# Optimization experiments

Measured on AMD Instinct MI355X. Metric: run time of the kernel, lower is better.

Reference implementation:

```python
import jax, jax.numpy as jnp
import numpy as np

N, L, S, D, H = 2, 2048, 2048, 128, 32  # batch, query len, state len, hidden_dim(=head dim), num_heads


def setup_inputs() -> dict:
    key = jax.random.key(0)
    ks = jax.random.split(key, 8)
    return {
        "query": jax.random.normal(ks[0], (N, L, D), dtype=jnp.float32),
        "states": jax.random.normal(ks[1], (N, S, D), dtype=jnp.float32),
        "Wk": jax.random.normal(ks[2], (H, D, D), dtype=jnp.float32) * 0.05,
        "bk": jax.random.normal(ks[3], (H, D), dtype=jnp.float32) * 0.05,
        "Wv": jax.random.normal(ks[4], (H, D, D), dtype=jnp.float32) * 0.05,
        "bv": jax.random.normal(ks[5], (H, D), dtype=jnp.float32) * 0.05,
        "Wc": jax.random.normal(ks[6], (H * D, D), dtype=jnp.float32) * 0.02,
        "bc": jax.random.normal(ks[7], (D,), dtype=jnp.float32) * 0.02,
    }


def reference(query, states, Wk, bk, Wv, bv, Wc, bc):
    # Per-head key/value projections (Attention.keys_mlp / values_mlp), batched over heads.
    K = jnp.einsum('nsd,hdk->nhsk', states, Wk) + bk[None, :, None, :]  # [N,H,S,D]
    V = jnp.einsum('nsd,hdk->nhsk', states, Wv) + bv[None, :, None, :]  # [N,H,S,D]
    scale = jnp.sqrt(jnp.asarray(K.shape[-1], query.dtype))
    logits = jnp.einsum('nld,nhsd->nhls', query, K) / scale            # [N,H,L,S]
    # Original detaches attention scores (softmax(...).detach()).
    A = jax.lax.stop_gradient(jax.nn.softmax(logits, axis=-1))
    ctx = jnp.einsum('nhls,nhsd->nhld', A, V)                          # [N,H,L,D]
    n, h, l, d = ctx.shape
    ctx = ctx.transpose(0, 2, 1, 3).reshape(n, l, h * d)               # concat heads -> [N,L,H*D]
    return ctx @ Wc + bc                                               # context_transform
```

## Files before the change

kernel.cpp:

```cpp
#include <hip/hip_runtime.h>
#include <hip/hip_bf16.h>

#define N_B 2
#define L_Q 2048
#define S_S 2048
#define D_D 128
#define H_H 32
#define SCALEK (0.08838834764831845f * 1.4426950408889634f)

typedef __attribute__((ext_vector_type(8))) short bf8;
typedef __attribute__((ext_vector_type(4))) short bf4;
typedef __attribute__((ext_vector_type(4))) float f4;

#define MFMA(a, b, c) __builtin_amdgcn_mfma_f32_16x16x32_bf16(a, b, c, 0, 0, 0)

__device__ __forceinline__ short f2bf(float x) {
    union { float f; unsigned u; } v; v.f = x;
    unsigned r = v.u + 0x7FFFu + ((v.u >> 16) & 1u);
    return (short)(r >> 16);
}

__device__ __forceinline__ bf4 pk4(float a, float b, float c, float d) {
    union { __hip_bfloat162 h2[2]; bf4 v; } u;
    u.h2[0] = __float22bfloat162_rn(make_float2(a, b));
    u.h2[1] = __float22bfloat162_rn(make_float2(c, d));
    return u.v;
}

__device__ __forceinline__ bf8 cat44(bf4 lo, bf4 hi) {
    bf8 r;
    r[0] = lo[0]; r[1] = lo[1]; r[2] = lo[2]; r[3] = lo[3];
    r[4] = hi[0]; r[5] = hi[1]; r[6] = hi[2]; r[7] = hi[3];
    return r;
}

__device__ __forceinline__ bf8 load8(const float* p) {
    const float4* q = (const float4*)p;
    float4 a = q[0], b = q[1];
    bf8 r;
    r[0] = f2bf(a.x); r[1] = f2bf(a.y); r[2] = f2bf(a.z); r[3] = f2bf(a.w);
    r[4] = f2bf(b.x); r[5] = f2bf(b.y); r[6] = f2bf(b.z); r[7] = f2bf(b.w);
    return r;
}

__device__ __forceinline__ void async16(const void* g, void* l) {
    __builtin_amdgcn_global_load_lds(
        (const __attribute__((address_space(1))) unsigned*)g,
        (__attribute__((address_space(3))) unsigned*)l, 16, 0, 0);
}

__global__ __launch_bounds__(256) void k_wct(const float* __restrict__ Wc,
                                             unsigned short* __restrict__ WcF) {
    int f16 = blockIdx.x * 256 + threadIdx.x;
    int l = f16 & 63, t = (f16 >> 6) & 3, nfA = (f16 >> 8) & 7, kc = f16 >> 11;
    int lrow = l & 15, lgrp = l >> 4;
    int kbase = kc * 128 + t * 32 + lgrp * 8;
    int n = nfA * 16 + lrow;
    bf8 v;
    #pragma unroll
    for (int j = 0; j < 8; ++j) v[j] = f2bf(Wc[(size_t)(kbase + j) * D_D + n]);
    *(bf8*)(WcF + (size_t)f16 * 8) = v;
}

__global__ __launch_bounds__(256) void k_wt(const float* __restrict__ Wk,
        const float* __restrict__ Wv, unsigned short* __restrict__ WkF,
        unsigned short* __restrict__ WvF) {
    __shared__ unsigned short T[128][129];
    const int tid = threadIdx.x;
    const int h = blockIdx.x;
    const int job = blockIdx.y;
    const float* W = (job ? Wv : Wk) + (size_t)h * (D_D * D_D);
    unsigned short* WF = (job ? WvF : WkF) + (size_t)h * (D_D * D_D);

    #pragma unroll
    for (int i = 0; i < 64; ++i) {
        int flat = i * 256 + tid;
        T[flat >> 7][flat & 127] = (unsigned short)f2bf(W[flat]);
    }
    __syncthreads();
    #pragma unroll
    for (int j8 = 0; j8 < 8; ++j8) {
        int f16 = j8 * 256 + tid;
        int l = f16 & 63, t = (f16 >> 6) & 3, df = (f16 >> 8) & 7;
        int lrow = l & 15, lgrp = l >> 4;
        bf8 v;
        #pragma unroll
        for (int j = 0; j < 8; ++j) v[j] = (short)T[t * 32 + lgrp * 8 + j][df * 16 + lrow];
        *(bf8*)(WF + (size_t)f16 * 8) = v;
    }
}

__global__ __launch_bounds__(256) void k_proj(const float* __restrict__ states,
        const unsigned short* __restrict__ WkF, const float* __restrict__ bk,
        const unsigned short* __restrict__ WvF, const float* __restrict__ bv,
        unsigned short* __restrict__ Kb, unsigned short* __restrict__ VTb) {
    const int tid = threadIdx.x;
    const int l = tid & 63, w = tid >> 6;
    const int lrow = l & 15, lgrp = l >> 4;
    const int bx = blockIdx.x;
    const int sc = bx & 31;
    const int nh = bx >> 5;
    const int h = nh & 31, n = nh >> 5;
    const int job = blockIdx.y;

    if (job == 0) {
        const unsigned short* WF = WkF + (size_t)h * (D_D * D_D);
        const float* srow = states + ((size_t)n * S_S + sc * 64 + w * 16 + lrow) * D_D;
        bf8 a[4];
        #pragma unroll
        for (int t = 0; t < 4; ++t) a[t] = load8(srow + t * 32 + lgrp * 8);
        f4 acc[8];
        #pragma unroll
        for (int i = 0; i < 8; ++i) acc[i] = (f4)(0.f);
        #pragma unroll
        for (int nf = 0; nf < 8; ++nf) {
            #pragma unroll
            for (int t = 0; t < 4; ++t) {
                bf8 b = *(const bf8*)(WF + (((nf * 4 + t) * 64 + l) << 3));
                acc[nf] = MFMA(a[t], b, acc[nf]);
            }
        }
        unsigned short* Kout = Kb + (size_t)(n * H_H + h) * S_S * D_D;
        #pragma unroll
        for (int nf = 0; nf < 8; ++nf) {
            int dcol = nf * 16 + lrow;
            float bias = bk[h * D_D + dcol];
            #pragma unroll
            for (int r = 0; r < 4; ++r) {
                int srw = sc * 64 + w * 16 + lgrp * 4 + r;
                Kout[(size_t)srw * D_D + dcol] = (unsigned short)f2bf((acc[nf][r] + bias) * SCALEK);
            }
        }
    } else {
        const unsigned short* WF = WvF + (size_t)h * (D_D * D_D);
        bf8 a[2][4];
        #pragma unroll
        for (int mf = 0; mf < 2; ++mf) {
            #pragma unroll
            for (int t = 0; t < 4; ++t)
                a[mf][t] = *(const bf8*)(WF + ((((w * 2 + mf) * 4 + t) * 64 + l) << 3));
        }
        f4 acc[2][4];
        #pragma unroll
        for (int mf = 0; mf < 2; ++mf)
            #pragma unroll
            for (int nf = 0; nf < 4; ++nf) acc[mf][nf] = (f4)(0.f);
        #pragma unroll
        for (int nf = 0; nf < 4; ++nf) {
            const float* srow = states + ((size_t)n * S_S + sc * 64 + nf * 16 + lrow) * D_D;
            #pragma unroll
            for (int t = 0; t < 4; ++t) {
                bf8 b = load8(srow + t * 32 + lgrp * 8);
                acc[0][nf] = MFMA(a[0][t], b, acc[0][nf]);
                acc[1][nf] = MFMA(a[1][t], b, acc[1][nf]);
            }
        }
        unsigned short* Vout = VTb + (size_t)(n * H_H + h) * D_D * S_S;
        #pragma unroll
        for (int mf = 0; mf < 2; ++mf) {
            #pragma unroll
            for (int r = 0; r < 4; ++r) {
                int drow = w * 32 + mf * 16 + lgrp * 4 + r;
                float bias = bv[h * D_D + drow];
                #pragma unroll
                for (int nf = 0; nf < 4; ++nf) {
                    int p = ((nf >> 1) << 5) + ((lrow >> 2) << 3) + ((nf & 1) << 2) + (lrow & 3);
                    int scol = sc * 64 + p;
                    Vout[(size_t)drow * S_S + scol] = (unsigned short)f2bf(acc[mf][nf][r] + bias);
                }
            }
        }
    }
}

__global__ __launch_bounds__(512) void k_attn(const float* __restrict__ query,
        const unsigned short* __restrict__ Kb, const unsigned short* __restrict__ VTb,
        unsigned short* __restrict__ CTX) {
    __shared__ char smem[65536];
    const int tid = threadIdx.x;
    const int l = tid & 63, w = tid >> 6;
    const int lrow = l & 15, lgrp = l >> 4;

    const int bid = blockIdx.x;
    const int bx = (bid & 7) * 64 + (bid >> 3);
    const int qt = bx & 7;
    const int nh = bx >> 3;
    const int h = nh & 31, n = nh >> 5;
    const int qbase = qt * 256 + w * 32;

    bf8 qf[2][4];
    #pragma unroll
    for (int mf = 0; mf < 2; ++mf) {
        const float* qp = query + ((size_t)n * L_Q + qbase + mf * 16 + lrow) * D_D;
        #pragma unroll
        for (int t = 0; t < 4; ++t) qf[mf][t] = load8(qp + t * 32 + lgrp * 8);
    }

    f4 oacc[2][8];
    #pragma unroll
    for (int mf = 0; mf < 2; ++mf)
        #pragma unroll
        for (int df = 0; df < 8; ++df) oacc[mf][df] = (f4)(0.f);
    float rsum[2] = {0.f, 0.f};

    const char* Kg = (const char*)(Kb + (size_t)(n * H_H + h) * S_S * D_D);
    const char* Vg = (const char*)(VTb + (size_t)(n * H_H + h) * D_D * S_S);

    auto stage = [&](int c, int sc2) {
        char* Kl = smem + c * 16384;
        char* Vl = smem + 32768 + c * 16384;
        #pragma unroll
        for (int i = 0; i < 2; ++i) {
            int kop = w * 2 + i;
            int o = kop * 1024 + l * 16;
            int r = o >> 8;
            int b = (o & 255) ^ ((r & 7) << 4);
            async16(Kg + (size_t)(sc2 * 64 + r) * 256 + b, Kl + kop * 1024);
        }
        #pragma unroll
        for (int i = 0; i < 2; ++i) {
            int vop = w * 2 + i;
            int o = vop * 1024 + l * 16;
            int r = o >> 7;
            int b = (o & 127) ^ ((r & 7) << 4);
            async16(Vg + (size_t)r * 4096 + sc2 * 128 + b, Vl + vop * 1024);
        }
    };

    auto iter = [&](int cur, int sc2, bool prefetch) {
        if (prefetch) stage(cur ^ 1, sc2 + 1);
        const char* Klds = smem + cur * 16384;
        const char* Vlds = smem + 32768 + cur * 16384;

        f4 sacc[2][4];
        #pragma unroll
        for (int mf = 0; mf < 2; ++mf)
            #pragma unroll
            for (int nf = 0; nf < 4; ++nf) sacc[mf][nf] = (f4)(0.f);
        __builtin_amdgcn_s_setprio(1);
        #pragma unroll
        for (int nf = 0; nf < 4; ++nf) {
            int srow = nf * 16 + lrow;
            int swz = (srow & 7) << 4;
            #pragma unroll
            for (int t = 0; t < 4; ++t) {
                bf8 kb = *(const bf8*)(Klds + srow * 256 + (((t * 32 + lgrp * 8) * 2) ^ swz));
                sacc[0][nf] = MFMA(kb, qf[0][t], sacc[0][nf]);
                sacc[1][nf] = MFMA(kb, qf[1][t], sacc[1][nf]);
            }
        }
        __builtin_amdgcn_s_setprio(0);

        bf8 pf[2][2];
        #pragma unroll
        for (int mf = 0; mf < 2; ++mf) {
            #pragma unroll
            for (int g = 0; g < 2; ++g) {
                bf4 pblk[2];
                #pragma unroll
                for (int b2 = 0; b2 < 2; ++b2) {
                    int nf = g * 2 + b2;
                    float p0 = __builtin_amdgcn_exp2f(sacc[mf][nf][0]);
                    float p1 = __builtin_amdgcn_exp2f(sacc[mf][nf][1]);
                    float p2 = __builtin_amdgcn_exp2f(sacc[mf][nf][2]);
                    float p3 = __builtin_amdgcn_exp2f(sacc[mf][nf][3]);
                    rsum[mf] += (p0 + p1) + (p2 + p3);
                    pblk[b2] = pk4(p0, p1, p2, p3);
                }
                pf[mf][g] = cat44(pblk[0], pblk[1]);
            }
        }

        __builtin_amdgcn_s_setprio(1);
        #pragma unroll
        for (int df = 0; df < 8; ++df) {
            int drow = df * 16 + lrow;
            int swz = (drow & 7) << 4;
            #pragma unroll
            for (int g = 0; g < 2; ++g) {
                bf8 vf = *(const bf8*)(Vlds + drow * 128 + ((g * 64 + lgrp * 16) ^ swz));
                oacc[0][df] = MFMA(vf, pf[0][g], oacc[0][df]);
                oacc[1][df] = MFMA(vf, pf[1][g], oacc[1][df]);
            }
        }
        __builtin_amdgcn_s_setprio(0);
        __syncthreads();
    };

    stage(0, 0);
    __syncthreads();
    for (int s2 = 0; s2 < 32; s2 += 2) {
        iter(0, s2, true);
        iter(1, s2 + 1, s2 + 1 < 31);
    }

    float rinv[2];
    #pragma unroll
    for (int mf = 0; mf < 2; ++mf) {
        float v = rsum[mf];
        v += __shfl_xor(v, 16, 64);
        v += __shfl_xor(v, 32, 64);
        rinv[mf] = 1.f / v;
    }
    #pragma unroll
    for (int mf = 0; mf < 2; ++mf) {
        int qrow = qbase + mf * 16 + lrow;
        unsigned short* crow = CTX + (size_t)(n * L_Q + qrow) * 4096 + h * D_D;
        #pragma unroll
        for (int df = 0; df < 8; ++df) {
            bf4 o = pk4(oacc[mf][df][0] * rinv[mf], oacc[mf][df][1] * rinv[mf],
                        oacc[mf][df][2] * rinv[mf], oacc[mf][df][3] * rinv[mf]);
            *(bf4*)(crow + df * 16 + lgrp * 4) = o;
        }
    }
}

__global__ __launch_bounds__(256) void k_out(const unsigned short* __restrict__ CTX,
        const unsigned short* __restrict__ WcF, const float* __restrict__ bc,
        float* __restrict__ out) {
    __shared__ char Alds[16384];
    const int tid = threadIdx.x;
    const int l = tid & 63, w = tid >> 6;
    const int lrow = l & 15, lgrp = l >> 4;
    const int m0 = blockIdx.x * 32;
    const char* Ag = (const char*)(CTX + (size_t)m0 * 4096);

    auto stage = [&](int c, int kc) {
        #pragma unroll
        for (int i = 0; i < 2; ++i) {
            int o = (w * 2 + i) * 1024 + l * 16;
            int r = o >> 8;
            int b = (o & 255) ^ ((r & 7) << 4);
            async16(Ag + (size_t)r * 8192 + kc * 256 + b, Alds + c * 8192 + (w * 2 + i) * 1024);
        }
    };

    f4 acc[2][2];
    #pragma unroll
    for (int mi = 0; mi < 2; ++mi) { acc[mi][0] = (f4)(0.f); acc[mi][1] = (f4)(0.f); }
    stage(0, 0);
    __syncthreads();
    int cur = 0;
    for (int kc = 0; kc < 32; ++kc) {
        if (kc < 31) stage(cur ^ 1, kc + 1);
        const char* Ac = Alds + cur * 8192;
        #pragma unroll
        for (int t = 0; t < 4; ++t) {
            int swz = (lrow & 7) << 4;
            int co = ((t * 32 + lgrp * 8) * 2) ^ swz;
            bf8 a0 = *(const bf8*)(Ac + lrow * 256 + co);
            bf8 a1 = *(const bf8*)(Ac + (16 + lrow) * 256 + co);
            #pragma unroll
            for (int nf = 0; nf < 2; ++nf) {
                int nfA = w * 2 + nf;
                bf8 b = *(const bf8*)(WcF + ((size_t)(((kc * 8 + nfA) * 4 + t) * 64 + l) << 3));
                acc[0][nf] = MFMA(a0, b, acc[0][nf]);
                acc[1][nf] = MFMA(a1, b, acc[1][nf]);
            }
        }
        __syncthreads();
        cur ^= 1;
    }
    #pragma unroll
    for (int mi = 0; mi < 2; ++mi) {
        #pragma unroll
        for (int nf = 0; nf < 2; ++nf) {
            int nc = w * 32 + nf * 16 + lrow;
            float bias = bc[nc];
            #pragma unroll
            for (int r = 0; r < 4; ++r)
                out[(size_t)(m0 + mi * 16 + lgrp * 4 + r) * D_D + nc] = acc[mi][nf][r] + bias;
        }
    }
}

extern "C" void kernel_launch(void* const* d_in, const int* in_sizes, int n_in,
                              void* d_out, int out_size, void* d_ws, size_t ws_size,
                              hipStream_t stream) {
    const float* query  = (const float*)d_in[0];
    const float* states = (const float*)d_in[1];
    const float* Wk = (const float*)d_in[2];
    const float* bk = (const float*)d_in[3];
    const float* Wv = (const float*)d_in[4];
    const float* bv = (const float*)d_in[5];
    const float* Wc = (const float*)d_in[6];
    const float* bc = (const float*)d_in[7];
    float* out = (float*)d_out;

    char* ws = (char*)d_ws;
    unsigned short* Kb  = (unsigned short*)(ws);
    unsigned short* VTb = (unsigned short*)(ws + 33554432);
    unsigned short* CTX = (unsigned short*)(ws + 67108864);
    unsigned short* WkF = (unsigned short*)(ws + 67108864);
    unsigned short* WvF = (unsigned short*)(ws + 67108864 + 1048576);
    unsigned short* WcF = (unsigned short*)(ws + 100663296);

    k_wct<<<256, 256, 0, stream>>>(Wc, WcF);
    dim3 gw(32, 2);
    k_wt<<<gw, 256, 0, stream>>>(Wk, Wv, WkF, WvF);
    dim3 gb(2048, 2);
    k_proj<<<gb, 256, 0, stream>>>(states, WkF, bk, WvF, bv, Kb, VTb);
    k_attn<<<512, 512, 0, stream>>>(query, Kb, VTb, CTX);
    k_out<<<128, 256, 0, stream>>>(CTX, WcF, bc, out);
}
```

Measured before the change: 226.9 us.

## Shrink attention tiles to 128 queries and 32-key chunks for higher occupancy

The attention kernel now runs 256-thread blocks covering 128 query rows and streams K/V in 32-key chunks instead of 64. Shared memory per block halves to 32KB, the grid doubles to 1024 blocks, and launch bounds request 4 blocks per CU. The V tile layout and swizzle are rewritten for the narrower chunk, and the loop runs 64 iterations. This aims for more resident waves and better latency hiding, at the cost of twice as many K/V loads per query row and more barriers per key processed.

```diff
diff --git a/kernel.cpp b/kernel.cpp
--- a/kernel.cpp
+++ b/kernel.cpp
@@ -173,20 +173,20 @@
     }
 }
 
-__global__ __launch_bounds__(512) void k_attn(const float* __restrict__ query,
+__global__ __launch_bounds__(256, 4) void k_attn(const float* __restrict__ query,
         const unsigned short* __restrict__ Kb, const unsigned short* __restrict__ VTb,
         unsigned short* __restrict__ CTX) {
-    __shared__ char smem[65536];
+    __shared__ char smem[32768];
     const int tid = threadIdx.x;
     const int l = tid & 63, w = tid >> 6;
     const int lrow = l & 15, lgrp = l >> 4;
 
     const int bid = blockIdx.x;
-    const int bx = (bid & 7) * 64 + (bid >> 3);
-    const int qt = bx & 7;
-    const int nh = bx >> 3;
+    const int bx = (bid & 7) * 128 + (bid >> 3);
+    const int qt = bx & 15;
+    const int nh = bx >> 4;
     const int h = nh & 31, n = nh >> 5;
-    const int qbase = qt * 256 + w * 32;
+    const int qbase = qt * 128 + w * 32;
 
     bf8 qf[2][4];
     #pragma unroll
@@ -207,39 +207,39 @@
     const char* Vg = (const char*)(VTb + (size_t)(n * H_H + h) * D_D * S_S);
 
     auto stage = [&](int c, int sc2) {
-        char* Kl = smem + c * 16384;
-        char* Vl = smem + 32768 + c * 16384;
+        char* Kl = smem + c * 8192;
+        char* Vl = smem + 16384 + c * 8192;
         #pragma unroll
         for (int i = 0; i < 2; ++i) {
             int kop = w * 2 + i;
             int o = kop * 1024 + l * 16;
             int r = o >> 8;
             int b = (o & 255) ^ ((r & 7) << 4);
-            async16(Kg + (size_t)(sc2 * 64 + r) * 256 + b, Kl + kop * 1024);
+            async16(Kg + (size_t)(sc2 * 32 + r) * 256 + b, Kl + kop * 1024);
         }
         #pragma unroll
         for (int i = 0; i < 2; ++i) {
             int vop = w * 2 + i;
             int o = vop * 1024 + l * 16;
-            int r = o >> 7;
-            int b = (o & 127) ^ ((r & 7) << 4);
-            async16(Vg + (size_t)r * 4096 + sc2 * 128 + b, Vl + vop * 1024);
+            int drow = o >> 6;
+            int b = (o & 63) ^ (((drow >> 1) & 3) << 4);
+            async16(Vg + (size_t)drow * 4096 + sc2 * 64 + b, Vl + vop * 1024);
         }
     };
 
     auto iter = [&](int cur, int sc2, bool prefetch) {
         if (prefetch) stage(cur ^ 1, sc2 + 1);
-        const char* Klds = smem + cur * 16384;
-        const char* Vlds = smem + 32768 + cur * 16384;
-
-        f4 sacc[2][4];
+        const char* Klds = smem + cur * 8192;
+        const char* Vlds = smem + 16384 + cur * 8192;
+
+        f4 sacc[2][2];
         #pragma unroll
         for (int mf = 0; mf < 2; ++mf)
             #pragma unroll
-            for (int nf = 0; nf < 4; ++nf) sacc[mf][nf] = (f4)(0.f);
+            for (int nf = 0; nf < 2; ++nf) sacc[mf][nf] = (f4)(0.f);
         __builtin_amdgcn_s_setprio(1);
         #pragma unroll
-        for (int nf = 0; nf < 4; ++nf) {
+        for (int nf = 0; nf < 2; ++nf) {
             int srow = nf * 16 + lrow;
             int swz = (srow & 7) << 4;
             #pragma unroll
@@ -251,37 +251,29 @@
         }
         __builtin_amdgcn_s_setprio(0);
 
-        bf8 pf[2][2];
+        bf8 pf[2];
         #pragma unroll
         for (int mf = 0; mf < 2; ++mf) {
-            #pragma unroll
-            for (int g = 0; g < 2; ++g) {
-                bf4 pblk[2];
-                #pragma unroll
-                for (int b2 = 0; b2 < 2; ++b2) {
-                    int nf = g * 2 + b2;
-                    float p0 = __builtin_amdgcn_exp2f(sacc[mf][nf][0]);
-                    float p1 = __builtin_amdgcn_exp2f(sacc[mf][nf][1]);
-                    float p2 = __builtin_amdgcn_exp2f(sacc[mf][nf][2]);
-                    float p3 = __builtin_amdgcn_exp2f(sacc[mf][nf][3]);
-                    rsum[mf] += (p0 + p1) + (p2 + p3);
-                    pblk[b2] = pk4(p0, p1, p2, p3);
-                }
-                pf[mf][g] = cat44(pblk[0], pblk[1]);
-            }
+            bf4 pblk[2];
+            #pragma unroll
+            for (int nf = 0; nf < 2; ++nf) {
+                float p0 = __builtin_amdgcn_exp2f(sacc[mf][nf][0]);
+                float p1 = __builtin_amdgcn_exp2f(sacc[mf][nf][1]);
+                float p2 = __builtin_amdgcn_exp2f(sacc[mf][nf][2]);
+                float p3 = __builtin_amdgcn_exp2f(sacc[mf][nf][3]);
+                rsum[mf] += (p0 + p1) + (p2 + p3);
+                pblk[nf] = pk4(p0, p1, p2, p3);
+            }
+            pf[mf] = cat44(pblk[0], pblk[1]);
         }
 
         __builtin_amdgcn_s_setprio(1);
         #pragma unroll
         for (int df = 0; df < 8; ++df) {
             int drow = df * 16 + lrow;
-            int swz = (drow & 7) << 4;
-            #pragma unroll
-            for (int g = 0; g < 2; ++g) {
-                bf8 vf = *(const bf8*)(Vlds + drow * 128 + ((g * 64 + lgrp * 16) ^ swz));
-                oacc[0][df] = MFMA(vf, pf[0][g], oacc[0][df]);
-                oacc[1][df] = MFMA(vf, pf[1][g], oacc[1][df]);
-            }
+            bf8 vf = *(const bf8*)(Vlds + drow * 64 + ((lgrp * 16) ^ (((drow >> 1) & 3) << 4)));
+            oacc[0][df] = MFMA(vf, pf[0], oacc[0][df]);
+            oacc[1][df] = MFMA(vf, pf[1], oacc[1][df]);
         }
         __builtin_amdgcn_s_setprio(0);
         __syncthreads();
@@ -289,9 +281,9 @@
 
     stage(0, 0);
     __syncthreads();
-    for (int s2 = 0; s2 < 32; s2 += 2) {
+    for (int s2 = 0; s2 < 64; s2 += 2) {
         iter(0, s2, true);
-        iter(1, s2 + 1, s2 + 1 < 31);
+        iter(1, s2 + 1, s2 + 1 < 63);
     }
 
     float rinv[2];
@@ -400,6 +392,6 @@
     k_wt<<<gw, 256, 0, stream>>>(Wk, Wv, WkF, WvF);
     dim3 gb(2048, 2);
     k_proj<<<gb, 256, 0, stream>>>(states, WkF, bk, WvF, bv, Kb, VTb);
-    k_attn<<<512, 512, 0, stream>>>(query, Kb, VTb, CTX);
+    k_attn<<<1024, 256, 0, stream>>>(query, Kb, VTb, CTX);
     k_out<<<128, 256, 0, stream>>>(CTX, WcF, bc, out);
 }
```

Result: slower. 634.2 us (+179.5%).
